# Kernel optimization log

Hardware: AMD Instinct MI355X
Metric: run time of the kernel (lower is better)

## Reference

```python
import jax, jax.numpy as jnp
import numpy as np

B, S, E = 8, 1024, 1024
MS = 128            # modal_context seq len
NH = 16             # attention heads
NE = 8              # total experts (4 shared + 4 modality-specific)
TOP_K = 2
FF = 4 * E          # expert hidden dim
EPS = 1e-5


def layer_norm(x, w, b, eps=EPS):
    m = jnp.mean(x, axis=-1, keepdims=True)
    v = jnp.mean(jnp.square(x - m), axis=-1, keepdims=True)
    return (x - m) / jnp.sqrt(v + eps) * w + b


def mha(q_in, kv_in, in_w, in_b, out_w, out_b, nh=NH):
    # torch nn.MultiheadAttention (batch_first) equivalent, eval mode (no dropout)
    e = q_in.shape[-1]
    q = q_in @ in_w[:e].T + in_b[:e]
    k = kv_in @ in_w[e:2 * e].T + in_b[e:2 * e]
    v = kv_in @ in_w[2 * e:].T + in_b[2 * e:]
    b, sq, _ = q.shape
    sk = k.shape[1]
    hd = e // nh
    q = q.reshape(b, sq, nh, hd).transpose(0, 2, 1, 3)
    k = k.reshape(b, sk, nh, hd).transpose(0, 2, 1, 3)
    v = v.reshape(b, sk, nh, hd).transpose(0, 2, 1, 3)
    scores = jnp.einsum('bhqd,bhkd->bhqk', q, k) * (1.0 / np.sqrt(hd).astype(np.float32))
    attn = jax.nn.softmax(scores, axis=-1)
    o = jnp.einsum('bhqk,bhkd->bhqd', attn, v).transpose(0, 2, 1, 3).reshape(b, sq, e)
    return o @ out_w.T + out_b


def _forward(x, modal_context,
             attn_in_w, attn_in_b, attn_out_w, attn_out_b,
             xattn_in_w, xattn_in_b, xattn_out_w, xattn_out_b,
             norm1_w, norm1_b, norm2_w, norm2_b, norm3_w, norm3_b,
             xnorm_w, xnorm_b, router_w, router_b, gate_w, gate_b,
             exp_ln_w, exp_ln_b, exp_fc1_w, exp_fc1_b, exp_fc2_w, exp_fc2_b):
    # --- self-attention block (pre-norm residual) ---
    h = x + mha(layer_norm(x, norm1_w, norm1_b), layer_norm(x, norm1_w, norm1_b),
                attn_in_w, attn_in_b, attn_out_w, attn_out_b)
    # --- cross-modal fusion with sigmoid modal gate ---
    xn = layer_norm(h, xnorm_w, xnorm_b)
    fusion = mha(xn, modal_context, xattn_in_w, xattn_in_b, xattn_out_w, xattn_out_b)
    gate = jax.nn.sigmoid(xn @ gate_w.T + gate_b)
    h = h + gate * fusion
    # --- MoE block: AttentiveRouter (softmax + top-k renorm) over shared+modality experts ---
    xn2 = layer_norm(h, norm2_w, norm2_b)
    logits = xn2 @ router_w.T + router_b                  # [B,S,NE]
    probs = jax.nn.softmax(logits, axis=-1)
    topw, topi = jax.lax.top_k(probs, TOP_K)              # [B,S,K]
    topw = topw / jnp.sum(topw, axis=-1, keepdims=True)
    # scatter top-k weights to dense combine tensor [B,S,NE]
    combine = jnp.sum(jax.nn.one_hot(topi, NE, dtype=x.dtype) * topw[..., None], axis=-2)
    moe = jnp.zeros_like(h)
    for e_idx in range(NE):  # small fixed loop over experts
        xe = layer_norm(xn2, exp_ln_w[e_idx], exp_ln_b[e_idx])
        hh = jax.nn.gelu(xe @ exp_fc1_w[e_idx].T + exp_fc1_b[e_idx])
        oe = hh @ exp_fc2_w[e_idx].T + exp_fc2_b[e_idx]
        moe = moe + combine[..., e_idx:e_idx + 1] * oe
    out = h + moe
    return layer_norm(out, norm3_w, norm3_b)


def setup_inputs() -> dict:
    key = jax.random.key(0)
    ks = jax.random.split(key, 32)
    std = 0.02
    d = {
        'x': jax.random.normal(ks[0], (B, S, E), jnp.float32),
        'modal_context': jax.random.normal(ks[1], (B, MS, E), jnp.float32),
        'attn_in_w': jax.random.normal(ks[2], (3 * E, E), jnp.float32) * std,
        'attn_in_b': jnp.zeros((3 * E,), jnp.float32),
        'attn_out_w': jax.random.normal(ks[3], (E, E), jnp.float32) * std,
        'attn_out_b': jnp.zeros((E,), jnp.float32),
        'xattn_in_w': jax.random.normal(ks[4], (3 * E, E), jnp.float32) * std,
        'xattn_in_b': jnp.zeros((3 * E,), jnp.float32),
        'xattn_out_w': jax.random.normal(ks[5], (E, E), jnp.float32) * std,
        'xattn_out_b': jnp.zeros((E,), jnp.float32),
        'norm1_w': jnp.ones((E,), jnp.float32), 'norm1_b': jnp.zeros((E,), jnp.float32),
        'norm2_w': jnp.ones((E,), jnp.float32), 'norm2_b': jnp.zeros((E,), jnp.float32),
        'norm3_w': jnp.ones((E,), jnp.float32), 'norm3_b': jnp.zeros((E,), jnp.float32),
        'xnorm_w': jnp.ones((E,), jnp.float32), 'xnorm_b': jnp.zeros((E,), jnp.float32),
        'router_w': jax.random.normal(ks[6], (NE, E), jnp.float32) * 0.1 / np.sqrt(E).astype(np.float32),
        'router_b': jnp.zeros((NE,), jnp.float32),
        'gate_w': jax.random.normal(ks[7], (E, E), jnp.float32) * std,
        'gate_b': jnp.zeros((E,), jnp.float32),
        'exp_ln_w': jnp.ones((NE, E), jnp.float32),
        'exp_ln_b': jnp.zeros((NE, E), jnp.float32),
        'exp_fc1_w': jax.random.normal(ks[8], (NE, FF, E), jnp.float32) * std,
        'exp_fc1_b': jnp.zeros((NE, FF), jnp.float32),
        'exp_fc2_w': jax.random.normal(ks[9], (NE, E, FF), jnp.float32) * std,
        'exp_fc2_b': jnp.zeros((NE, E), jnp.float32),
    }
    return d


def reference(x, modal_context,
              attn_in_w, attn_in_b, attn_out_w, attn_out_b,
              xattn_in_w, xattn_in_b, xattn_out_w, xattn_out_b,
              norm1_w, norm1_b, norm2_w, norm2_b, norm3_w, norm3_b,
              xnorm_w, xnorm_b, router_w, router_b, gate_w, gate_b,
              exp_ln_w, exp_ln_b, exp_fc1_w, exp_fc1_b, exp_fc2_w, exp_fc2_b):
    return _forward(x, modal_context,
                    attn_in_w, attn_in_b, attn_out_w, attn_out_b,
                    xattn_in_w, xattn_in_b, xattn_out_w, xattn_out_b,
                    norm1_w, norm1_b, norm2_w, norm2_b, norm3_w, norm3_b,
                    xnorm_w, xnorm_b, router_w, router_b, gate_w, gate_b,
                    exp_ln_w, exp_ln_b, exp_fc1_w, exp_fc1_b, exp_fc2_w, exp_fc2_b)
```

## Files before the change

kernel.cpp:

```cpp
#include <hip/hip_runtime.h>
#include <cstdint>
#include <cstddef>
#include <math.h>

typedef unsigned short u16;
typedef __attribute__((ext_vector_type(4))) float f32x4;
typedef __attribute__((ext_vector_type(8))) short short8;
typedef __attribute__((ext_vector_type(4))) short short4v;

__device__ __forceinline__ float b2f(u16 u) {
    union { unsigned int i; float f; } v; v.i = ((unsigned int)u) << 16; return v.f;
}
__device__ __forceinline__ u16 f2b(float f) {
    union { float f; unsigned int i; } v; v.f = f;
    unsigned int i = v.i;
    return (u16)((i + 0x7FFFu + ((i >> 16) & 1u)) >> 16);
}
__device__ __forceinline__ void split3t(float a, short& h, short& m, short& l) {
    union { float f; unsigned int u; } va, vh, v1, vm, v2;
    va.f = a;
    vh.u = va.u & 0xFFFF0000u;
    float r1 = a - vh.f;
    v1.f = r1;
    vm.u = v1.u & 0xFFFF0000u;
    float r2 = r1 - vm.f;
    v2.f = r2;
    h = (short)(vh.u >> 16);
    m = (short)(vm.u >> 16);
    l = (short)(v2.u >> 16);
}
__device__ __forceinline__ float gelu_f(float x) {
    float x3 = x * x * x;
    float y = 0.7978845608028654f * (x + 0.044715f * x3);
    float ya = fminf(fabsf(y), 15.f);
    float e = expf(-2.f * ya);
    float t = (1.f - e) / (1.f + e);
    t = copysignf(t, y);
    return 0.5f * x * (1.f + t);
}
__device__ __forceinline__ void gld16(const u16* g, u16* l)
{
    __builtin_amdgcn_global_load_lds(
        (const __attribute__((address_space(1))) void*)(g),
        (__attribute__((address_space(3))) void*)(l),
        16, 0, 0);
}

struct EGemmP {
    const float* A; int lda; long aSo, aSi; int aDiv;
    const float* B; int ldb; long bSo, bSi; int bDiv;
    float* C; int ldc; long cSo, cSi; int cDiv;
    const float* bias;
    const float* resid;
    const float* fus;
    int K;
};

template<int EPI, int WM, int WN, int MF, int NF>
__global__ __launch_bounds__(256)
void gemm_emu(EGemmP p)
{
    constexpr int TM = WM * MF * 16;
    constexpr int TN = WN * NF * 16;
    constexpr int TK = 32;
    __shared__ u16 Ah[TM * TK], Am[TM * TK], Al[TM * TK];
    __shared__ u16 Bh[TN * TK], Bm[TN * TK], Bl[TN * TK];
    const int tid = threadIdx.x;
    const int z = blockIdx.z;
    const float* Ab = p.A + (long)(z / p.aDiv) * p.aSo + (long)(z % p.aDiv) * p.aSi
                      + (long)blockIdx.x * TM * p.lda;
    const float* Bb = p.B + (long)(z / p.bDiv) * p.bSo + (long)(z % p.bDiv) * p.bSi
                      + (long)blockIdx.y * TN * p.ldb;
    const int lane = tid & 63;
    const int wv = tid >> 6;
    const int wm = wv / WN;
    const int wn = wv % WN;
    const int kg = lane >> 4;
    const int l16 = lane & 15;
    f32x4 acc[MF][NF];
#pragma unroll
    for (int m = 0; m < MF; ++m)
#pragma unroll
        for (int n = 0; n < NF; ++n)
            acc[m][n] = (f32x4){0.f, 0.f, 0.f, 0.f};

    for (int k0 = 0; k0 < p.K; k0 += TK) {
#pragma unroll
        for (int i = 0; i < (TM * TK) / 1024; ++i) {
            int e = i * 256 + tid;
            int r = e >> 3;
            int c = (e & 7) * 4;
            f32x4 a = *(const f32x4*)&Ab[(long)r * p.lda + k0 + c];
            short4v h, m, l;
#pragma unroll
            for (int j = 0; j < 4; ++j) {
                short th, tm2, tl2;
                split3t(a[j], th, tm2, tl2);
                h[j] = th; m[j] = tm2; l[j] = tl2;
            }
            *(short4v*)&Ah[r * TK + c] = h;
            *(short4v*)&Am[r * TK + c] = m;
            *(short4v*)&Al[r * TK + c] = l;
        }
#pragma unroll
        for (int i = 0; i < (TN * TK) / 1024; ++i) {
            int e = i * 256 + tid;
            int r = e >> 3;
            int c = (e & 7) * 4;
            f32x4 a = *(const f32x4*)&Bb[(long)r * p.ldb + k0 + c];
            short4v h, m, l;
#pragma unroll
            for (int j = 0; j < 4; ++j) {
                short th, tm2, tl2;
                split3t(a[j], th, tm2, tl2);
                h[j] = th; m[j] = tm2; l[j] = tl2;
            }
            *(short4v*)&Bh[r * TK + c] = h;
            *(short4v*)&Bm[r * TK + c] = m;
            *(short4v*)&Bl[r * TK + c] = l;
        }
        __syncthreads();
        short8 ah[MF], am[MF], al[MF], bh[NF], bm[NF], bl[NF];
#pragma unroll
        for (int m = 0; m < MF; ++m) {
            int ro = (wm * MF * 16 + m * 16 + l16) * TK + kg * 8;
            ah[m] = *(const short8*)&Ah[ro];
            am[m] = *(const short8*)&Am[ro];
            al[m] = *(const short8*)&Al[ro];
        }
#pragma unroll
        for (int n = 0; n < NF; ++n) {
            int ro = (wn * NF * 16 + n * 16 + l16) * TK + kg * 8;
            bh[n] = *(const short8*)&Bh[ro];
            bm[n] = *(const short8*)&Bm[ro];
            bl[n] = *(const short8*)&Bl[ro];
        }
#pragma unroll
        for (int m = 0; m < MF; ++m)
#pragma unroll
            for (int n = 0; n < NF; ++n) {
                f32x4 a = acc[m][n];
                a = __builtin_amdgcn_mfma_f32_16x16x32_bf16(al[m], bh[n], a, 0, 0, 0);
                a = __builtin_amdgcn_mfma_f32_16x16x32_bf16(ah[m], bl[n], a, 0, 0, 0);
                a = __builtin_amdgcn_mfma_f32_16x16x32_bf16(am[m], bm[n], a, 0, 0, 0);
                a = __builtin_amdgcn_mfma_f32_16x16x32_bf16(am[m], bh[n], a, 0, 0, 0);
                a = __builtin_amdgcn_mfma_f32_16x16x32_bf16(ah[m], bm[n], a, 0, 0, 0);
                a = __builtin_amdgcn_mfma_f32_16x16x32_bf16(ah[m], bh[n], a, 0, 0, 0);
                acc[m][n] = a;
            }
        __syncthreads();
    }
    const long cbase = (long)(z / p.cDiv) * p.cSo + (long)(z % p.cDiv) * p.cSi;
#pragma unroll
    for (int m = 0; m < MF; ++m)
#pragma unroll
        for (int n = 0; n < NF; ++n) {
            const int colt = blockIdx.y * TN + wn * NF * 16 + n * 16 + l16;
            float bv = p.bias ? p.bias[colt] : 0.f;
#pragma unroll
            for (int r = 0; r < 4; ++r) {
                const int rowt = blockIdx.x * TM + wm * MF * 16 + m * 16 + kg * 4 + r;
                const long idx = cbase + (long)rowt * p.ldc + colt;
                float v = acc[m][n][r] + bv;
                if constexpr (EPI == 0) {
                    p.C[idx] = v;
                } else if constexpr (EPI == 1) {
                    p.C[idx] = v + p.resid[idx];
                } else {
                    float g = 1.f / (1.f + expf(-v));
                    p.C[idx] = p.resid[idx] + g * p.fus[idx];
                }
            }
        }
}

struct MoeP {
    const u16* A; int lda;
    const u16* Bw; long bStrideE; int ldb;
    u16* HHo;
    float* M1; float* M2;
    int ldc;
    const float* biasE; long biasStride;
    const float* combine;
    const int* cnt;
    const int* pfx;
    const int* tlist;
    int K;
};

template<int EPI>
__global__ __launch_bounds__(256)
void gemm_moe(MoeP p)
{
    const int ex = blockIdx.z;
    const int count = p.cnt[ex];
    if ((int)(blockIdx.x * 128) >= count) return;
    const int base = p.pfx[ex];
    constexpr int TK = 64;
    __shared__ __align__(16) u16 lA[128 * TK];
    __shared__ __align__(16) u16 lB[128 * TK];
    const int tid = threadIdx.x;
    const u16* Ab = p.A + (long)(base + blockIdx.x * 128) * p.lda;
    const u16* Bb = p.Bw + (long)ex * p.bStrideE + (long)blockIdx.y * 128 * p.ldb;
    const int lane = tid & 63;
    const int wv = tid >> 6;
    const int wm = wv >> 1;
    const int wn = wv & 1;
    const int kg = lane >> 4;
    const int l16 = lane & 15;
    f32x4 acc[4][4];
#pragma unroll
    for (int m = 0; m < 4; ++m)
#pragma unroll
        for (int n = 0; n < 4; ++n)
            acc[m][n] = (f32x4){0.f, 0.f, 0.f, 0.f};

    for (int k0 = 0; k0 < p.K; k0 += TK) {
#pragma unroll
        for (int i = 0; i < 4; ++i) {
            int e = i * 256 + tid;
            int r = e >> 3;
            int jg = (e & 7) ^ (r & 7);
            gld16(&Ab[(long)r * p.lda + k0 + jg * 8], &lA[e * 8]);
            gld16(&Bb[(long)r * p.ldb + k0 + jg * 8], &lB[e * 8]);
        }
        __syncthreads();
#pragma unroll
        for (int ks = 0; ks < 2; ++ks) {
            short8 af[4], bfr[4];
#pragma unroll
            for (int m = 0; m < 4; ++m) {
                int row = wm * 64 + m * 16 + l16;
                int jj = (ks * 4 + kg) ^ (row & 7);
                af[m] = *(const short8*)&lA[row * TK + jj * 8];
            }
#pragma unroll
            for (int n = 0; n < 4; ++n) {
                int row = wn * 64 + n * 16 + l16;
                int jj = (ks * 4 + kg) ^ (row & 7);
                bfr[n] = *(const short8*)&lB[row * TK + jj * 8];
            }
#pragma unroll
            for (int m = 0; m < 4; ++m)
#pragma unroll
                for (int n = 0; n < 4; ++n)
                    acc[m][n] = __builtin_amdgcn_mfma_f32_16x16x32_bf16(af[m], bfr[n], acc[m][n], 0, 0, 0);
        }
        __syncthreads();
    }
    const float* bias = p.biasE + (long)ex * p.biasStride;
#pragma unroll
    for (int m = 0; m < 4; ++m)
#pragma unroll
        for (int n = 0; n < 4; ++n) {
            const int colt = blockIdx.y * 128 + wn * 64 + n * 16 + l16;
            const float bv = bias[colt];
#pragma unroll
            for (int r = 0; r < 4; ++r) {
                const int rowt = blockIdx.x * 128 + wm * 64 + m * 16 + kg * 4 + r;
                if (rowt >= count) continue;
                float v = acc[m][n][r] + bv;
                if constexpr (EPI == 3) {
                    p.HHo[(long)(base + rowt) * p.ldc + colt] = f2b(gelu_f(v));
                } else {
                    const int entry = p.tlist[ex * 8192 + rowt];
                    const int tok = entry & 0xFFFF;
                    const int k = entry >> 16;
                    const float w = p.combine[(long)tok * 8 + ex];
                    float* dst = k ? p.M2 : p.M1;
                    dst[(long)tok * p.ldc + colt] = w * v;
                }
            }
        }
}

template<int MODE>
__global__ __launch_bounds__(256)
void ln2p(const float* in, const float* add1, const float* add2,
          const float* w, const float* b, float* outf)
{
    const long row = blockIdx.x;
    const int t = threadIdx.x;
    const int c0 = t * 4;
    f32x4 v = *(const f32x4*)&in[row * 1024 + c0];
    if constexpr (MODE == 2) {
        f32x4 a1 = *(const f32x4*)&add1[row * 1024 + c0];
        f32x4 a2 = *(const f32x4*)&add2[row * 1024 + c0];
#pragma unroll
        for (int j = 0; j < 4; ++j) v[j] += a1[j] + a2[j];
    }
    __shared__ float r1[4], r2[4];
    const int lane = t & 63, wv = t >> 6;
    float s1 = v[0] + v[1] + v[2] + v[3];
    for (int o = 32; o; o >>= 1) s1 += __shfl_xor(s1, o);
    if (lane == 0) r1[wv] = s1;
    __syncthreads();
    const float mean = (r1[0] + r1[1] + r1[2] + r1[3]) * (1.f / 1024.f);
    f32x4 d;
#pragma unroll
    for (int j = 0; j < 4; ++j) d[j] = v[j] - mean;
    float s2 = d[0] * d[0] + d[1] * d[1] + d[2] * d[2] + d[3] * d[3];
    for (int o = 32; o; o >>= 1) s2 += __shfl_xor(s2, o);
    if (lane == 0) r2[wv] = s2;
    __syncthreads();
    const float var = (r2[0] + r2[1] + r2[2] + r2[3]) * (1.f / 1024.f);
    const float rstd = 1.f / sqrtf(var + 1e-5f);
    f32x4 o4;
#pragma unroll
    for (int j = 0; j < 4; ++j) o4[j] = d[j] * rstd * w[c0 + j] + b[c0 + j];
    *(f32x4*)&outf[row * 1024 + c0] = o4;
}

__global__ __launch_bounds__(256)
void rowstats(const float* in, float* st, int* cnt)
{
    if (blockIdx.x == 0 && threadIdx.x < 8) cnt[threadIdx.x] = 0;
    const long row = blockIdx.x;
    const int t = threadIdx.x;
    const int c0 = t * 4;
    f32x4 v = *(const f32x4*)&in[row * 1024 + c0];
    __shared__ float r1[4], r2[4];
    const int lane = t & 63, wv = t >> 6;
    float s1 = v[0] + v[1] + v[2] + v[3];
    for (int o = 32; o; o >>= 1) s1 += __shfl_xor(s1, o);
    if (lane == 0) r1[wv] = s1;
    __syncthreads();
    const float mean = (r1[0] + r1[1] + r1[2] + r1[3]) * (1.f / 1024.f);
    float s2 = 0.f;
#pragma unroll
    for (int j = 0; j < 4; ++j) { float d = v[j] - mean; s2 += d * d; }
    for (int o = 32; o; o >>= 1) s2 += __shfl_xor(s2, o);
    if (lane == 0) r2[wv] = s2;
    __syncthreads();
    if (t == 0) {
        const float var = (r2[0] + r2[1] + r2[2] + r2[3]) * (1.f / 1024.f);
        st[row * 2] = mean;
        st[row * 2 + 1] = 1.f / sqrtf(var + 1e-5f);
    }
}

__global__ __launch_bounds__(256)
void softmax_f32(float* sm, int C, float scale)
{
    const long row = blockIdx.x;
    float* p = sm + row * (long)C;
    const int t = threadIdx.x;
    const int idx = t * 4;
    const bool act = idx < C;
    f32x4 v = (f32x4){-1e30f, -1e30f, -1e30f, -1e30f};
    if (act) {
        v = *(const f32x4*)&p[idx];
#pragma unroll
        for (int j = 0; j < 4; ++j) v[j] *= scale;
    }
    float mx = fmaxf(fmaxf(v[0], v[1]), fmaxf(v[2], v[3]));
    for (int o = 32; o; o >>= 1) mx = fmaxf(mx, __shfl_xor(mx, o));
    __shared__ float red[4], red2[4];
    const int lane = t & 63, wv = t >> 6;
    if (lane == 0) red[wv] = mx;
    __syncthreads();
    mx = fmaxf(fmaxf(red[0], red[1]), fmaxf(red[2], red[3]));
    float e[4], s = 0.f;
    if (act) {
#pragma unroll
        for (int j = 0; j < 4; ++j) { e[j] = expf(v[j] - mx); s += e[j]; }
    }
    for (int o = 32; o; o >>= 1) s += __shfl_xor(s, o);
    if (lane == 0) red2[wv] = s;
    __syncthreads();
    s = red2[0] + red2[1] + red2[2] + red2[3];
    if (act) {
        f32x4 o4;
#pragma unroll
        for (int j = 0; j < 4; ++j) o4[j] = e[j] / s;
        *(f32x4*)&p[idx] = o4;
    }
}

__global__ __launch_bounds__(256)
void transpose64f(const float* src, int sld, long sSo, long sSi, int sDiv, float* dst, int Skv)
{
    const int z = blockIdx.y;
    const float* Sp = src + (long)(z / sDiv) * sSo + (long)(z % sDiv) * sSi;
    float* Dp = dst + (long)z * 64 * Skv;
    const int j0 = blockIdx.x * 64;
    __shared__ float tl[64][68];
    const int tid = threadIdx.x;
#pragma unroll
    for (int it = 0; it < 4; ++it) {
        int e = (it * 256 + tid) * 4;
        int r = e >> 6, c = e & 63;
        f32x4 d = *(const f32x4*)&Sp[(long)(j0 + r) * sld + c];
        *(f32x4*)&tl[r][c] = d;
    }
    __syncthreads();
    const int d0 = tid >> 2;
    const int jc = (tid & 3) * 16;
    float tmp[16];
#pragma unroll
    for (int i = 0; i < 16; ++i) tmp[i] = tl[jc + i][d0];
#pragma unroll
    for (int i = 0; i < 16; ++i) Dp[(long)d0 * Skv + j0 + jc + i] = tmp[i];
}

__global__ __launch_bounds__(256)
void router_k(const float* xn2, const float* rw, const float* rb, float* cmb,
              int* cnt, int* tlist)
{
    const int tok = blockIdx.x * 4 + (threadIdx.x >> 6);
    const int lane = threadIdx.x & 63;
    const float* xp = xn2 + (long)tok * 1024 + lane * 16;
    float xv[16];
#pragma unroll
    for (int j = 0; j < 16; ++j) xv[j] = xp[j];
    double acc[8];
#pragma unroll
    for (int e = 0; e < 8; ++e) {
        const float* wp = rw + e * 1024 + lane * 16;
        double s = 0.0;
#pragma unroll
        for (int j = 0; j < 16; ++j) s += (double)xv[j] * (double)wp[j];
        acc[e] = s;
    }
    for (int o = 32; o; o >>= 1) {
#pragma unroll
        for (int e = 0; e < 8; ++e) acc[e] += __shfl_xor(acc[e], o);
    }
    if (lane == 0) {
        double l[8];
#pragma unroll
        for (int e = 0; e < 8; ++e) l[e] = acc[e] + (double)rb[e];
        int i1 = 0;
#pragma unroll
        for (int e = 1; e < 8; ++e) if (l[e] > l[i1]) i1 = e;
        int i2 = (i1 == 0) ? 1 : 0;
#pragma unroll
        for (int e = 0; e < 8; ++e) if (e != i1 && l[e] > l[i2]) i2 = e;
        double w1 = 1.0 / (1.0 + exp(l[i2] - l[i1]));
        double w2 = 1.0 - w1;
        float c8[8] = {0, 0, 0, 0, 0, 0, 0, 0};
        c8[i1] = (float)w1;
        c8[i2] = (float)w2;
        float* cp = cmb + (long)tok * 8;
#pragma unroll
        for (int e = 0; e < 8; ++e) cp[e] = c8[e];
        int s1 = atomicAdd(&cnt[i1], 1);
        tlist[i1 * 8192 + s1] = tok;
        int s2 = atomicAdd(&cnt[i2], 1);
        tlist[i2 * 8192 + s2] = tok | 65536;
    }
}

__global__ void prefix8(const int* cnt, int* pfx)
{
    if (threadIdx.x == 0) {
        int s = 0;
#pragma unroll
        for (int e = 0; e < 8; ++e) { pfx[e] = s; s += cnt[e]; }
    }
}

__global__ __launch_bounds__(256)
void gather_all(const float* xn2, const float* st, const int* cnt, const int* pfx,
                const int* tlist, const float* lnw, const float* lnb, u16* xe)
{
    const int e = blockIdx.y;
    const int slot = blockIdx.x;
    if (slot >= cnt[e]) return;
    const int tok = tlist[e * 8192 + slot] & 0xFFFF;
    const int c0 = threadIdx.x * 4;
    f32x4 v = *(const f32x4*)&xn2[(long)tok * 1024 + c0];
    const float m = st[tok * 2], r = st[tok * 2 + 1];
    const float* w = lnw + (long)e * 1024;
    const float* b = lnb + (long)e * 1024;
    short4v o4;
#pragma unroll
    for (int j = 0; j < 4; ++j) o4[j] = (short)f2b((v[j] - m) * r * w[c0 + j] + b[c0 + j]);
    *(short4v*)&xe[(long)(pfx[e] + slot) * 1024 + c0] = o4;
}

__global__ __launch_bounds__(256)
void cvtw(const float* in, u16* out, long n4)
{
    const long stride = (long)gridDim.x * 256;
    for (long i = (long)blockIdx.x * 256 + threadIdx.x; i < n4; i += stride) {
        f32x4 v = *(const f32x4*)&in[i * 4];
        short4v o;
#pragma unroll
        for (int j = 0; j < 4; ++j) o[j] = (short)f2b(v[j]);
        *(short4v*)&out[i * 4] = o;
    }
}

extern "C" void kernel_launch(void* const* d_in, const int* in_sizes, int n_in,
                              void* d_out, int out_size, void* d_ws, size_t ws_size,
                              hipStream_t stream)
{
    (void)in_sizes; (void)n_in; (void)out_size;
    const float* x          = (const float*)d_in[0];
    const float* modal      = (const float*)d_in[1];
    const float* attn_in_w  = (const float*)d_in[2];
    const float* attn_in_b  = (const float*)d_in[3];
    const float* attn_out_w = (const float*)d_in[4];
    const float* attn_out_b = (const float*)d_in[5];
    const float* xattn_in_w = (const float*)d_in[6];
    const float* xattn_in_b = (const float*)d_in[7];
    const float* xattn_out_w= (const float*)d_in[8];
    const float* xattn_out_b= (const float*)d_in[9];
    const float* norm1_w = (const float*)d_in[10];
    const float* norm1_b = (const float*)d_in[11];
    const float* norm2_w = (const float*)d_in[12];
    const float* norm2_b = (const float*)d_in[13];
    const float* norm3_w = (const float*)d_in[14];
    const float* norm3_b = (const float*)d_in[15];
    const float* xnorm_w = (const float*)d_in[16];
    const float* xnorm_b = (const float*)d_in[17];
    const float* router_w = (const float*)d_in[18];
    const float* router_b = (const float*)d_in[19];
    const float* gate_w = (const float*)d_in[20];
    const float* gate_b = (const float*)d_in[21];
    const float* exp_ln_w = (const float*)d_in[22];
    const float* exp_ln_b = (const float*)d_in[23];
    const float* exp_fc1_w = (const float*)d_in[24];
    const float* exp_fc1_b = (const float*)d_in[25];
    const float* exp_fc2_w = (const float*)d_in[26];
    const float* exp_fc2_b = (const float*)d_in[27];

    char* wsb = (char*)d_ws;
    size_t off = 0;
    auto AL = [&](size_t bytes) { size_t r = off; off += (bytes + 255) & ~(size_t)255; return r; };
    float* XN  = (float*)(wsb + AL(33554432));
    float* H   = (float*)(wsb + AL(33554432));
    float* H2  = (float*)(wsb + AL(33554432));
    float* XN2 = (float*)(wsb + AL(33554432));
    float* FUS = (float*)(wsb + AL(33554432));
    float* MOE = (float*)(wsb + AL(33554432));
    float* XKV = (float*)(wsb + AL(8388608));
    float* CMB = (float*)(wsb + AL(262144));
    float* ST  = (float*)(wsb + AL(65536));
    int*   CNT = (int*)(wsb + AL(256));
    int*   PFX = (int*)(wsb + AL(256));
    int*   TLS = (int*)(wsb + AL(262144));
    char*  RA  = wsb + AL(100663296);
    char*  RB  = wsb + AL(100663296);
    if (off > ws_size) return;

    float* QKV = (float*)RA;
    float* XQ  = (float*)RA;
    float* XO  = (float*)(RA + 33554432);
    float* SCf = (float*)RB;
    float* VTf = (float*)(RB + 67108864);
    u16*   HH  = (u16*)RA;
    u16*   XE  = (u16*)(RA + 135266304);
    u16*   WB  = (u16*)XN;
    float* out = (float*)d_out;

    ln2p<0><<<8192, 256, 0, stream>>>(x, nullptr, nullptr, norm1_w, norm1_b, XN);

    {
        EGemmP p{XN, 1024, 0, 0, 1, attn_in_w, 1024, 0, 0, 1,
                 QKV, 3072, 0, 0, 1, attn_in_b, nullptr, nullptr, 1024};
        gemm_emu<0, 2, 2, 4, 2><<<dim3(64, 48, 1), 256, 0, stream>>>(p);
    }
    transpose64f<<<dim3(16, 128), 256, 0, stream>>>(QKV + 2048, 3072, (long)1024 * 3072, 64, 16, VTf, 1024);

    for (int g = 0; g < 8; ++g) {
        EGemmP s{QKV + (long)g * 1024 * 3072, 3072, 0, 64, 16,
                 QKV + 1024 + (long)g * 1024 * 3072, 3072, 0, 64, 16,
                 SCf, 1024, 0, (long)1024 * 1024, 16, nullptr, nullptr, nullptr, 64};
        gemm_emu<0, 2, 2, 4, 2><<<dim3(8, 16, 16), 256, 0, stream>>>(s);

        softmax_f32<<<16 * 1024, 256, 0, stream>>>(SCf, 1024, 0.125f);

        EGemmP v{SCf, 1024, 0, (long)1024 * 1024, 16,
                 VTf + (long)g * 16 * 64 * 1024, 1024, 0, (long)64 * 1024, 16,
                 XN + (long)g * 1024 * 1024, 1024, 0, 64, 16, nullptr, nullptr, nullptr, 1024};
        gemm_emu<0, 2, 2, 2, 2><<<dim3(16, 1, 16), 256, 0, stream>>>(v);
    }

    {
        EGemmP p{XN, 1024, 0, 0, 1, attn_out_w, 1024, 0, 0, 1,
                 H, 1024, 0, 0, 1, attn_out_b, x, nullptr, 1024};
        gemm_emu<1, 2, 2, 4, 2><<<dim3(64, 16, 1), 256, 0, stream>>>(p);
    }
    ln2p<0><<<8192, 256, 0, stream>>>(H, nullptr, nullptr, xnorm_w, xnorm_b, XN);

    {
        EGemmP p{XN, 1024, 0, 0, 1, xattn_in_w, 1024, 0, 0, 1,
                 XQ, 1024, 0, 0, 1, xattn_in_b, nullptr, nullptr, 1024};
        gemm_emu<0, 2, 2, 4, 2><<<dim3(64, 16, 1), 256, 0, stream>>>(p);
    }
    {
        EGemmP p{modal, 1024, 0, 0, 1, xattn_in_w + (size_t)1024 * 1024, 1024, 0, 0, 1,
                 XKV, 2048, 0, 0, 1, xattn_in_b + 1024, nullptr, nullptr, 1024};
        gemm_emu<0, 2, 2, 4, 2><<<dim3(8, 32, 1), 256, 0, stream>>>(p);
    }
    transpose64f<<<dim3(2, 128), 256, 0, stream>>>(XKV + 1024, 2048, (long)128 * 2048, 64, 16, VTf, 128);

    {
        EGemmP s{XQ, 1024, (long)1024 * 1024, 64, 16,
                 XKV, 2048, (long)128 * 2048, 64, 16,
                 SCf, 128, 0, (long)1024 * 128, 1 << 20, nullptr, nullptr, nullptr, 64};
        gemm_emu<0, 2, 2, 4, 2><<<dim3(8, 2, 128), 256, 0, stream>>>(s);
    }
    softmax_f32<<<128 * 1024, 256, 0, stream>>>(SCf, 128, 0.125f);
    {
        EGemmP v{SCf, 128, 0, (long)1024 * 128, 1 << 20,
                 VTf, 128, 0, (long)64 * 128, 1 << 20,
                 XO, 1024, (long)1024 * 1024, 64, 16, nullptr, nullptr, nullptr, 128};
        gemm_emu<0, 2, 2, 4, 2><<<dim3(8, 1, 128), 256, 0, stream>>>(v);
    }
    {
        EGemmP p{XO, 1024, 0, 0, 1, xattn_out_w, 1024, 0, 0, 1,
                 FUS, 1024, 0, 0, 1, xattn_out_b, nullptr, nullptr, 1024};
        gemm_emu<0, 2, 2, 4, 2><<<dim3(64, 16, 1), 256, 0, stream>>>(p);
    }
    {
        EGemmP p{XN, 1024, 0, 0, 1, gate_w, 1024, 0, 0, 1,
                 H2, 1024, 0, 0, 1, gate_b, H, FUS, 1024};
        gemm_emu<2, 2, 2, 4, 2><<<dim3(64, 16, 1), 256, 0, stream>>>(p);
    }
    ln2p<0><<<8192, 256, 0, stream>>>(H2, nullptr, nullptr, norm2_w, norm2_b, XN2);
    rowstats<<<8192, 256, 0, stream>>>(XN2, ST, CNT);
    router_k<<<2048, 256, 0, stream>>>(XN2, router_w, router_b, CMB, CNT, TLS);
    prefix8<<<1, 64, 0, stream>>>(CNT, PFX);

    gather_all<<<dim3(8192, 8), 256, 0, stream>>>(XN2, ST, CNT, PFX, TLS, exp_ln_w, exp_ln_b, XE);
    cvtw<<<2048, 256, 0, stream>>>(exp_fc1_w, WB, 8388608);
    {
        MoeP p1{XE, 1024, WB, (long)4096 * 1024, 1024,
                HH, nullptr, nullptr, 4096,
                exp_fc1_b, 4096, nullptr, CNT, PFX, TLS, 1024};
        gemm_moe<3><<<dim3(64, 32, 8), 256, 0, stream>>>(p1);
    }
    cvtw<<<2048, 256, 0, stream>>>(exp_fc2_w, WB, 8388608);
    {
        MoeP p2{HH, 4096, WB, (long)1024 * 4096, 4096,
                nullptr, MOE, FUS, 1024,
                exp_fc2_b, 1024, CMB, CNT, PFX, TLS, 4096};
        gemm_moe<4><<<dim3(64, 8, 8), 256, 0, stream>>>(p2);
    }

    ln2p<2><<<8192, 256, 0, stream>>>(H2, MOE, FUS, norm3_w, norm3_b, out);
}
```

Measured before the change: 2.853 ms.

## Pre-split QKV projection operands into bf16 planes and use 128x128 MFMA GEMM

The QKV input projection now splits the layernormed activations and the in-projection weights once into three bf16 planes (high/mid/low) with a separate kernel. It then runs a new 128x128-tile GEMM that loads the planes straight into shared memory with a swizzled layout and does six bf16 MFMAs per fragment pair. Before, the emulated-fp32 GEMM presumably split operands inside its inner loop. This removes repeated splitting work and raises per-tile reuse, at the cost of extra memory traffic for the split planes and two more kernel launches.

```diff
diff --git a/kernel.cpp b/kernel.cpp
--- a/kernel.cpp
+++ b/kernel.cpp
@@ -172,6 +172,117 @@
                 }
             }
         }
+}
+
+struct PlP {
+    const u16* Ap; long aPS; int lda;
+    const u16* Bp; long bPS; int ldb;
+    float* C; int ldc;
+    const float* bias;
+    int K;
+};
+
+__global__ __launch_bounds__(256)
+void gemm_pl(PlP p)
+{
+    constexpr int TK = 32;
+    __shared__ __align__(16) u16 sAh[128 * TK], sAm[128 * TK], sAl[128 * TK];
+    __shared__ __align__(16) u16 sBh[128 * TK], sBm[128 * TK], sBl[128 * TK];
+    const int tid = threadIdx.x;
+    const int lane = tid & 63;
+    const int wv = tid >> 6;
+    const int wm = wv >> 1;
+    const int wn = wv & 1;
+    const int kg = lane >> 4;
+    const int l16 = lane & 15;
+    const u16* Ab = p.Ap + (long)blockIdx.x * 128 * p.lda;
+    const u16* Bb = p.Bp + (long)blockIdx.y * 128 * p.ldb;
+    f32x4 acc[4][4];
+#pragma unroll
+    for (int m = 0; m < 4; ++m)
+#pragma unroll
+        for (int n = 0; n < 4; ++n)
+            acc[m][n] = (f32x4){0.f, 0.f, 0.f, 0.f};
+
+    for (int k0 = 0; k0 < p.K; k0 += TK) {
+#pragma unroll
+        for (int i = 0; i < 2; ++i) {
+            int e = i * 256 + tid;
+            int r = e >> 2;
+            int jg = (e & 3) ^ (r & 3) ^ ((r >> 2) & 3);
+            long ga = (long)r * p.lda + k0 + jg * 8;
+            long gb = (long)r * p.ldb + k0 + jg * 8;
+            gld16(&Ab[ga],            &sAh[e * 8]);
+            gld16(&Ab[ga + p.aPS],    &sAm[e * 8]);
+            gld16(&Ab[ga + 2 * p.aPS],&sAl[e * 8]);
+            gld16(&Bb[gb],            &sBh[e * 8]);
+            gld16(&Bb[gb + p.bPS],    &sBm[e * 8]);
+            gld16(&Bb[gb + 2 * p.bPS],&sBl[e * 8]);
+        }
+        __syncthreads();
+        short8 ah[4], am[4], al[4];
+#pragma unroll
+        for (int m = 0; m < 4; ++m) {
+            int row = wm * 64 + m * 16 + l16;
+            int slot = kg ^ (row & 3) ^ ((row >> 2) & 3);
+            int idx = row * TK + slot * 8;
+            ah[m] = *(const short8*)&sAh[idx];
+            am[m] = *(const short8*)&sAm[idx];
+            al[m] = *(const short8*)&sAl[idx];
+        }
+#pragma unroll
+        for (int n = 0; n < 4; ++n) {
+            int row = wn * 64 + n * 16 + l16;
+            int slot = kg ^ (row & 3) ^ ((row >> 2) & 3);
+            int idx = row * TK + slot * 8;
+            short8 bh = *(const short8*)&sBh[idx];
+            short8 bm = *(const short8*)&sBm[idx];
+            short8 bl = *(const short8*)&sBl[idx];
+#pragma unroll
+            for (int m = 0; m < 4; ++m) {
+                f32x4 a = acc[m][n];
+                a = __builtin_amdgcn_mfma_f32_16x16x32_bf16(al[m], bh, a, 0, 0, 0);
+                a = __builtin_amdgcn_mfma_f32_16x16x32_bf16(ah[m], bl, a, 0, 0, 0);
+                a = __builtin_amdgcn_mfma_f32_16x16x32_bf16(am[m], bm, a, 0, 0, 0);
+                a = __builtin_amdgcn_mfma_f32_16x16x32_bf16(am[m], bh, a, 0, 0, 0);
+                a = __builtin_amdgcn_mfma_f32_16x16x32_bf16(ah[m], bm, a, 0, 0, 0);
+                a = __builtin_amdgcn_mfma_f32_16x16x32_bf16(ah[m], bh, a, 0, 0, 0);
+                acc[m][n] = a;
+            }
+        }
+        __syncthreads();
+    }
+#pragma unroll
+    for (int m = 0; m < 4; ++m)
+#pragma unroll
+        for (int n = 0; n < 4; ++n) {
+            const int colt = blockIdx.y * 128 + wn * 64 + n * 16 + l16;
+            const float bv = p.bias ? p.bias[colt] : 0.f;
+#pragma unroll
+            for (int r = 0; r < 4; ++r) {
+                const int rowt = blockIdx.x * 128 + wm * 64 + m * 16 + kg * 4 + r;
+                p.C[(long)rowt * p.ldc + colt] = acc[m][n][r] + bv;
+            }
+        }
+}
+
+__global__ __launch_bounds__(256)
+void splitp(const float* in, u16* out, long pstride, long n4)
+{
+    const long stride = (long)gridDim.x * 256;
+    for (long i = (long)blockIdx.x * 256 + threadIdx.x; i < n4; i += stride) {
+        f32x4 v = *(const f32x4*)&in[i * 4];
+        short4v h, m, l;
+#pragma unroll
+        for (int j = 0; j < 4; ++j) {
+            short th, tm2, tl2;
+            split3t(v[j], th, tm2, tl2);
+            h[j] = th; m[j] = tm2; l[j] = tl2;
+        }
+        *(short4v*)&out[i * 4] = h;
+        *(short4v*)&out[pstride + i * 4] = m;
+        *(short4v*)&out[2 * pstride + i * 4] = l;
+    }
 }
 
 struct MoeP {
@@ -553,14 +664,18 @@
     u16*   HH  = (u16*)RA;
     u16*   XE  = (u16*)(RA + 135266304);
     u16*   WB  = (u16*)XN;
+    u16*   APq = (u16*)H2;
+    u16*   WPq = (u16*)FUS;
     float* out = (float*)d_out;
 
     ln2p<0><<<8192, 256, 0, stream>>>(x, nullptr, nullptr, norm1_w, norm1_b, XN);
-
-    {
-        EGemmP p{XN, 1024, 0, 0, 1, attn_in_w, 1024, 0, 0, 1,
-                 QKV, 3072, 0, 0, 1, attn_in_b, nullptr, nullptr, 1024};
-        gemm_emu<0, 2, 2, 4, 2><<<dim3(64, 48, 1), 256, 0, stream>>>(p);
+    splitp<<<2048, 256, 0, stream>>>(XN, APq, (long)8192 * 1024, 2097152);
+    splitp<<<2048, 256, 0, stream>>>(attn_in_w, WPq, (long)3072 * 1024, 786432);
+
+    {
+        PlP p{APq, (long)8192 * 1024, 1024, WPq, (long)3072 * 1024, 1024,
+              QKV, 3072, attn_in_b, 1024};
+        gemm_pl<<<dim3(64, 24), 256, 0, stream>>>(p);
     }
     transpose64f<<<dim3(16, 128), 256, 0, stream>>>(QKV + 2048, 3072, (long)1024 * 3072, 64, 16, VTf, 1024);
 
```

Measured after the change: 2.874 ms. About the same (+0.7%).
